# Optimization experiments

Hardware: AMD Instinct MI355X
Metric: run time of the kernel (lower is better)

## Reference

```python
import jax, jax.numpy as jnp
import numpy as np

NEG_INF = -1e9  # matches torch masked_fill value -1000000000.0
K = 3  # Conv1d kernel size


def setup_inputs() -> dict:
    key = jax.random.key(0)
    k1, k2, k3, k4 = jax.random.split(key, 4)
    B, V, F, H = 128, 200, 64, 128
    input_visit = jax.random.normal(k1, (B, V, F), dtype=jnp.float32)
    visit_mask = jax.random.randint(k2, (B, 1, V - K + 1), 0, 2, dtype=jnp.int32)
    # per-feature Conv1d(1, H, 3) weights stacked: [F, H, K], bias [F, H]
    fan_in = 1 * K
    bound = 1.0 / np.sqrt(fan_in)
    conv_w = jax.random.uniform(k3, (F, H, K), dtype=jnp.float32, minval=-bound, maxval=bound)
    conv_b = jax.random.uniform(k4, (F, H), dtype=jnp.float32, minval=-bound, maxval=bound)
    return {"input_visit": input_visit, "visit_mask": visit_mask, "conv_w": conv_w, "conv_b": conv_b}


def reference(input_visit, visit_mask, conv_w, conv_b):
    # input_visit: [B, V, F]; visit_mask: [B, 1, L] with L = V-K+1
    B, V, F = input_visit.shape
    L = V - K + 1
    x = jnp.transpose(input_visit, (0, 2, 1))  # [B, F, V]
    # sliding windows: [B, F, L, K]
    win = jnp.stack([x[:, :, k:k + L] for k in range(K)], axis=-1)
    # per-feature conv (in_channels=1): [B, F, H, L]
    conv = jnp.einsum('bflk,fhk->bfhl', win, conv_w) + conv_b[None, :, :, None]
    # masked_fill where mask == 0, broadcast [B,1,1,L] -> [B,F,H,L]
    masked = jnp.where(visit_mask[:, None, :, :] == 0, NEG_INF, conv)
    # max over time -> [B, F, H] (== torch.cat of per-feature outputs along dim=1)
    return jnp.max(masked, axis=-1)
```

## Files before the change

kernel.cpp:

```cpp
#include <hip/hip_runtime.h>


#define NEG_INF_F (-1e9f)

typedef float v2f __attribute__((ext_vector_type(2)));

constexpr int B_ = 128;
constexpr int V_ = 200;
constexpr int F_ = 64;
constexpr int H_ = 128;
constexpr int L_ = V_ - 3 + 1;

constexpr int NTHR = 256;
constexpr int FG   = 8;
constexpr int HPT  = 8;
constexpr int MAXW = (L_ + 7) & ~7;
constexpr int WSTR = 4 * MAXW + 8;

__global__ __launch_bounds__(NTHR)
void fve_kernel(const float* __restrict__ x,
                const int*   __restrict__ mask,
                const float* __restrict__ w,
                const float* __restrict__ bias,
                float* __restrict__ out)
{
    __shared__ __align__(16) float xc[FG][WSTR];
    __shared__ int vlist[L_];
    __shared__ int vcnt;

    const int b  = blockIdx.x >> 3;
    const int f0 = (blockIdx.x & 7) * FG;
    const int t  = threadIdx.x;

    if (t == 0) vcnt = 0;
    __syncthreads();

    if (t < L_ && mask[b * L_ + t] != 0) {
        const int p = atomicAdd(&vcnt, 1);
        vlist[p] = t;
    }
    __syncthreads();

    const int n    = vcnt;
    const int npad = (n + 7) & ~7;

    for (int item = t; item < npad * 8; item += NTHR) {
        const int j    = item >> 3;
        const int k    = (item >> 1) & 3;
        const int half = item & 1;
        if (k == 3) continue;
        const int l = (j < n) ? vlist[j] : vlist[0];
        const float4 g = *reinterpret_cast<const float4*>(
            x + ((size_t)b * V_ + l + k) * F_ + f0 + half * 4);
        const int col = 4 * j + k;
        xc[half * 4 + 0][col] = g.x;
        xc[half * 4 + 1][col] = g.y;
        xc[half * 4 + 2][col] = g.z;
        xc[half * 4 + 3][col] = g.w;
    }
    __syncthreads();

    const int f_local = t >> 5;
    const int f       = f0 + f_local;
    const int h_lane  = (t >> 1) & 15;
    const int h0      = h_lane * HPT;
    const int l_lane  = t & 1;

    const float* wp = w + ((size_t)f * H_ + h0) * 3;
    float wt[24];
#pragma unroll
    for (int j = 0; j < 6; ++j)
        *reinterpret_cast<float4*>(&wt[j * 4]) =
            *reinterpret_cast<const float4*>(wp + j * 4);

    float bsc[8];
    *reinterpret_cast<float4*>(&bsc[0]) =
        *reinterpret_cast<const float4*>(bias + (size_t)f * H_ + h0);
    *reinterpret_cast<float4*>(&bsc[4]) =
        *reinterpret_cast<const float4*>(bias + (size_t)f * H_ + h0 + 4);

    v2f wp0[4], wp1[4], wp2[4], bpk[4], mpk[4];
#pragma unroll
    for (int p = 0; p < 4; ++p) {
        wp0[p] = (v2f){wt[6 * p + 0], wt[6 * p + 3]};
        wp1[p] = (v2f){wt[6 * p + 1], wt[6 * p + 4]};
        wp2[p] = (v2f){wt[6 * p + 2], wt[6 * p + 5]};
        bpk[p] = (v2f){bsc[2 * p], bsc[2 * p + 1]};
        mpk[p] = (v2f){NEG_INF_F, NEG_INF_F};
    }

    const float4* xq = reinterpret_cast<const float4*>(&xc[f_local][0]);

#define PROCQ(Q)                                                              \
    do {                                                                      \
        const v2f X0 = (v2f){(Q).x, (Q).x};                                   \
        const v2f X1 = (v2f){(Q).y, (Q).y};                                   \
        const v2f X2 = (v2f){(Q).z, (Q).z};                                   \
        _Pragma("unroll")                                                     \
        for (int p = 0; p < 4; ++p) {                                         \
            const v2f c = __builtin_elementwise_fma(X0, wp0[p],               \
                          __builtin_elementwise_fma(X1, wp1[p],               \
                          __builtin_elementwise_fma(X2, wp2[p], bpk[p])));    \
            mpk[p] = __builtin_elementwise_max(mpk[p], c);                    \
        }                                                                     \
    } while (0)

    for (int u = 0; u < npad; u += 8) {
        const int i0 = u + l_lane;
        const float4 q0 = xq[i0];
        const float4 q1 = xq[i0 + 2];
        const float4 q2 = xq[i0 + 4];
        const float4 q3 = xq[i0 + 6];
        PROCQ(q0);
        PROCQ(q1);
        PROCQ(q2);
        PROCQ(q3);
    }
#undef PROCQ

#pragma unroll
    for (int p = 0; p < 4; ++p) {
        const float a = __shfl_xor(mpk[p].x, 1, 64);
        const float c = __shfl_xor(mpk[p].y, 1, 64);
        mpk[p].x = fmaxf(mpk[p].x, a);
        mpk[p].y = fmaxf(mpk[p].y, c);
    }

    float* op = out + ((size_t)b * F_ + f) * H_ + h0 + l_lane * 4;
    const int pb = l_lane * 2;
    *reinterpret_cast<float4*>(op) =
        make_float4(mpk[pb].x, mpk[pb].y, mpk[pb + 1].x, mpk[pb + 1].y);
}

extern "C" void kernel_launch(void* const* d_in, const int* in_sizes, int n_in,
                              void* d_out, int out_size, void* d_ws, size_t ws_size,
                              hipStream_t stream) {
    const float* x    = (const float*)d_in[0];
    const int*   mask = (const int*)d_in[1];
    const float* w    = (const float*)d_in[2];
    const float* bias = (const float*)d_in[3];
    float* out = (float*)d_out;

    const int grid = B_ * (F_ / FG);
    fve_kernel<<<grid, NTHR, 0, stream>>>(x, mask, w, bias, out);
}
```

Before: 16.20 us.

## Double features per block and h-outputs per thread for more register reuse

Each block now handles 16 features instead of 8, so the grid shrinks to 512 blocks and each gathered x window feeds more features. Each thread computes 16 h-channels instead of 8, so every LDS float4 load is reused across twice as many FMAs. Each wave now covers 4 features with 8 h-lanes and 2 l-lanes. The costs are more registers per thread, fewer blocks to spread across CUs, and more shared memory per block, all of which can lower occupancy.

```diff
diff --git a/kernel.cpp b/kernel.cpp
--- a/kernel.cpp
+++ b/kernel.cpp
@@ -12,8 +12,9 @@
 constexpr int L_ = V_ - 3 + 1;
 
 constexpr int NTHR = 256;
-constexpr int FG   = 8;
-constexpr int HPT  = 8;
+constexpr int FG   = 16;
+constexpr int NFW  = 4;
+constexpr int HPT  = 16;
 constexpr int MAXW = (L_ + 7) & ~7;
 constexpr int WSTR = 4 * MAXW + 8;
 
@@ -28,8 +29,8 @@
     __shared__ int vlist[L_];
     __shared__ int vcnt;
 
-    const int b  = blockIdx.x >> 3;
-    const int f0 = (blockIdx.x & 7) * FG;
+    const int b  = blockIdx.x >> 2;
+    const int f0 = (blockIdx.x & 3) * FG;
     const int t  = threadIdx.x;
 
     if (t == 0) vcnt = 0;
@@ -44,44 +45,47 @@
     const int n    = vcnt;
     const int npad = (n + 7) & ~7;
 
-    for (int item = t; item < npad * 8; item += NTHR) {
-        const int j    = item >> 3;
-        const int k    = (item >> 1) & 3;
-        const int half = item & 1;
+    for (int item = t; item < npad * 16; item += NTHR) {
+        const int j = item >> 4;
+        const int k = (item >> 2) & 3;
+        const int q = item & 3;
         if (k == 3) continue;
         const int l = (j < n) ? vlist[j] : vlist[0];
         const float4 g = *reinterpret_cast<const float4*>(
-            x + ((size_t)b * V_ + l + k) * F_ + f0 + half * 4);
+            x + ((size_t)b * V_ + l + k) * F_ + f0 + q * 4);
         const int col = 4 * j + k;
-        xc[half * 4 + 0][col] = g.x;
-        xc[half * 4 + 1][col] = g.y;
-        xc[half * 4 + 2][col] = g.z;
-        xc[half * 4 + 3][col] = g.w;
+        xc[4 * q + 0][col] = g.x;
+        xc[4 * q + 1][col] = g.y;
+        xc[4 * q + 2][col] = g.z;
+        xc[4 * q + 3][col] = g.w;
     }
     __syncthreads();
 
-    const int f_local = t >> 5;
+    const int wave    = t >> 6;
+    const int lane    = t & 63;
+    const int f_sub   = lane >> 4;
+    const int h_lane  = (lane >> 1) & 7;
+    const int l_lane  = lane & 1;
+    const int f_local = wave * NFW + f_sub;
     const int f       = f0 + f_local;
-    const int h_lane  = (t >> 1) & 15;
     const int h0      = h_lane * HPT;
-    const int l_lane  = t & 1;
 
     const float* wp = w + ((size_t)f * H_ + h0) * 3;
-    float wt[24];
+    float wt[48];
 #pragma unroll
-    for (int j = 0; j < 6; ++j)
+    for (int j = 0; j < 12; ++j)
         *reinterpret_cast<float4*>(&wt[j * 4]) =
             *reinterpret_cast<const float4*>(wp + j * 4);
 
-    float bsc[8];
-    *reinterpret_cast<float4*>(&bsc[0]) =
-        *reinterpret_cast<const float4*>(bias + (size_t)f * H_ + h0);
-    *reinterpret_cast<float4*>(&bsc[4]) =
-        *reinterpret_cast<const float4*>(bias + (size_t)f * H_ + h0 + 4);
+    float bsc[16];
+#pragma unroll
+    for (int j = 0; j < 4; ++j)
+        *reinterpret_cast<float4*>(&bsc[j * 4]) =
+            *reinterpret_cast<const float4*>(bias + (size_t)f * H_ + h0 + j * 4);
 
-    v2f wp0[4], wp1[4], wp2[4], bpk[4], mpk[4];
+    v2f wp0[8], wp1[8], wp2[8], bpk[8], mpk[8];
 #pragma unroll
-    for (int p = 0; p < 4; ++p) {
+    for (int p = 0; p < 8; ++p) {
         wp0[p] = (v2f){wt[6 * p + 0], wt[6 * p + 3]};
         wp1[p] = (v2f){wt[6 * p + 1], wt[6 * p + 4]};
         wp2[p] = (v2f){wt[6 * p + 2], wt[6 * p + 5]};
@@ -97,7 +101,7 @@
         const v2f X1 = (v2f){(Q).y, (Q).y};                                   \
         const v2f X2 = (v2f){(Q).z, (Q).z};                                   \
         _Pragma("unroll")                                                     \
-        for (int p = 0; p < 4; ++p) {                                         \
+        for (int p = 0; p < 8; ++p) {                                         \
             const v2f c = __builtin_elementwise_fma(X0, wp0[p],               \
                           __builtin_elementwise_fma(X1, wp1[p],               \
                           __builtin_elementwise_fma(X2, wp2[p], bpk[p])));    \
@@ -119,17 +123,19 @@
 #undef PROCQ
 
 #pragma unroll
-    for (int p = 0; p < 4; ++p) {
+    for (int p = 0; p < 8; ++p) {
         const float a = __shfl_xor(mpk[p].x, 1, 64);
         const float c = __shfl_xor(mpk[p].y, 1, 64);
         mpk[p].x = fmaxf(mpk[p].x, a);
         mpk[p].y = fmaxf(mpk[p].y, c);
     }
 
-    float* op = out + ((size_t)b * F_ + f) * H_ + h0 + l_lane * 4;
-    const int pb = l_lane * 2;
+    float* op = out + ((size_t)b * F_ + f) * H_ + h0 + l_lane * 8;
+    const int pb = l_lane * 4;
     *reinterpret_cast<float4*>(op) =
         make_float4(mpk[pb].x, mpk[pb].y, mpk[pb + 1].x, mpk[pb + 1].y);
+    *reinterpret_cast<float4*>(op + 4) =
+        make_float4(mpk[pb + 2].x, mpk[pb + 2].y, mpk[pb + 3].x, mpk[pb + 3].y);
 }
 
 extern "C" void kernel_launch(void* const* d_in, const int* in_sizes, int n_in,
```

After: 18.30 us. +13.0%, slower.

## Widen per-thread H tile, hoist weight loads, use ballot-based mask compaction

Applied to the files above, without the earlier changes.

Each thread now computes 16 output channels instead of 8, with four lanes splitting the time steps, so every shared-memory read of a window feeds twice as many FMAs. The weight and bias global loads are moved ahead of the first barrier so their latency overlaps the mask compaction. Mask compaction now uses a wavefront ballot plus one atomic per wave instead of one atomic per valid position. The trade-off is roughly double the per-thread register use, padding to 16 positions, and an extra shuffle round in the final max reduction.

```diff
diff --git a/kernel.cpp b/kernel.cpp
--- a/kernel.cpp
+++ b/kernel.cpp
@@ -13,9 +13,9 @@
 
 constexpr int NTHR = 256;
 constexpr int FG   = 8;
-constexpr int HPT  = 8;
-constexpr int MAXW = (L_ + 7) & ~7;
-constexpr int WSTR = 4 * MAXW + 8;
+constexpr int HPT  = 16;
+constexpr int MAXW = (L_ + 15) & ~15;
+constexpr int WSTR = 4 * MAXW + 16;
 
 __global__ __launch_bounds__(NTHR)
 void fve_kernel(const float* __restrict__ x,
@@ -25,24 +25,53 @@
                 float* __restrict__ out)
 {
     __shared__ __align__(16) float xc[FG][WSTR];
-    __shared__ int vlist[L_];
+    __shared__ int vlist[MAXW];
     __shared__ int vcnt;
 
     const int b  = blockIdx.x >> 3;
     const int f0 = (blockIdx.x & 7) * FG;
     const int t  = threadIdx.x;
+    const int lane = t & 63;
+
+    const int f_sub   = lane >> 5;
+    const int h_lane  = (lane >> 2) & 7;
+    const int l_lane  = lane & 3;
+    const int f_local = (t >> 6) * 2 + f_sub;
+    const int f       = f0 + f_local;
+    const int h0      = h_lane * HPT;
 
     if (t == 0) vcnt = 0;
+
+    const float* wp = w + ((size_t)f * H_ + h0) * 3;
+    float wt[48];
+#pragma unroll
+    for (int j = 0; j < 12; ++j)
+        *reinterpret_cast<float4*>(&wt[j * 4]) =
+            *reinterpret_cast<const float4*>(wp + j * 4);
+
+    float bsc[16];
+#pragma unroll
+    for (int j = 0; j < 4; ++j)
+        *reinterpret_cast<float4*>(&bsc[j * 4]) =
+            *reinterpret_cast<const float4*>(bias + (size_t)f * H_ + h0 + j * 4);
+
     __syncthreads();
 
-    if (t < L_ && mask[b * L_ + t] != 0) {
-        const int p = atomicAdd(&vcnt, 1);
-        vlist[p] = t;
+    {
+        const bool valid = (t < L_) && (mask[b * L_ + t] != 0);
+        const unsigned long long bal = __ballot(valid);
+        int base = 0;
+        if (lane == 0) base = atomicAdd(&vcnt, __popcll(bal));
+        base = __shfl(base, 0, 64);
+        if (valid) {
+            const int pos = base + (int)__popcll(bal & ((1ull << lane) - 1ull));
+            vlist[pos] = t;
+        }
     }
     __syncthreads();
 
     const int n    = vcnt;
-    const int npad = (n + 7) & ~7;
+    const int npad = (n + 15) & ~15;
 
     for (int item = t; item < npad * 8; item += NTHR) {
         const int j    = item >> 3;
@@ -60,28 +89,9 @@
     }
     __syncthreads();
 
-    const int f_local = t >> 5;
-    const int f       = f0 + f_local;
-    const int h_lane  = (t >> 1) & 15;
-    const int h0      = h_lane * HPT;
-    const int l_lane  = t & 1;
-
-    const float* wp = w + ((size_t)f * H_ + h0) * 3;
-    float wt[24];
+    v2f wp0[8], wp1[8], wp2[8], bpk[8], mpk[8];
 #pragma unroll
-    for (int j = 0; j < 6; ++j)
-        *reinterpret_cast<float4*>(&wt[j * 4]) =
-            *reinterpret_cast<const float4*>(wp + j * 4);
-
-    float bsc[8];
-    *reinterpret_cast<float4*>(&bsc[0]) =
-        *reinterpret_cast<const float4*>(bias + (size_t)f * H_ + h0);
-    *reinterpret_cast<float4*>(&bsc[4]) =
-        *reinterpret_cast<const float4*>(bias + (size_t)f * H_ + h0 + 4);
-
-    v2f wp0[4], wp1[4], wp2[4], bpk[4], mpk[4];
-#pragma unroll
-    for (int p = 0; p < 4; ++p) {
+    for (int p = 0; p < 8; ++p) {
         wp0[p] = (v2f){wt[6 * p + 0], wt[6 * p + 3]};
         wp1[p] = (v2f){wt[6 * p + 1], wt[6 * p + 4]};
         wp2[p] = (v2f){wt[6 * p + 2], wt[6 * p + 5]};
@@ -97,7 +107,7 @@
         const v2f X1 = (v2f){(Q).y, (Q).y};                                   \
         const v2f X2 = (v2f){(Q).z, (Q).z};                                   \
         _Pragma("unroll")                                                     \
-        for (int p = 0; p < 4; ++p) {                                         \
+        for (int p = 0; p < 8; ++p) {                                         \
             const v2f c = __builtin_elementwise_fma(X0, wp0[p],               \
                           __builtin_elementwise_fma(X1, wp1[p],               \
                           __builtin_elementwise_fma(X2, wp2[p], bpk[p])));    \
@@ -105,12 +115,12 @@
         }                                                                     \
     } while (0)
 
-    for (int u = 0; u < npad; u += 8) {
+    for (int u = 0; u < npad; u += 16) {
         const int i0 = u + l_lane;
         const float4 q0 = xq[i0];
-        const float4 q1 = xq[i0 + 2];
-        const float4 q2 = xq[i0 + 4];
-        const float4 q3 = xq[i0 + 6];
+        const float4 q1 = xq[i0 + 4];
+        const float4 q2 = xq[i0 + 8];
+        const float4 q3 = xq[i0 + 12];
         PROCQ(q0);
         PROCQ(q1);
         PROCQ(q2);
@@ -119,9 +129,13 @@
 #undef PROCQ
 
 #pragma unroll
-    for (int p = 0; p < 4; ++p) {
-        const float a = __shfl_xor(mpk[p].x, 1, 64);
-        const float c = __shfl_xor(mpk[p].y, 1, 64);
+    for (int p = 0; p < 8; ++p) {
+        float a = __shfl_xor(mpk[p].x, 1, 64);
+        float c = __shfl_xor(mpk[p].y, 1, 64);
+        mpk[p].x = fmaxf(mpk[p].x, a);
+        mpk[p].y = fmaxf(mpk[p].y, c);
+        a = __shfl_xor(mpk[p].x, 2, 64);
+        c = __shfl_xor(mpk[p].y, 2, 64);
         mpk[p].x = fmaxf(mpk[p].x, a);
         mpk[p].y = fmaxf(mpk[p].y, c);
     }
```

Result: slower. 18.31 us (+13.1%).

## Halve features per block, split time across four lanes, use ballot compaction

Applied to the files above, without the earlier changes.

Each block now handles 4 features instead of 8, which doubles the grid to 2048 blocks. Each wave owns one feature, and four lanes split the time axis between them, with a two-step shuffle max at the end. The shared-memory atomic compaction of valid timesteps is replaced by a wave ballot/popcount prefix scan, and launch bounds request 8 blocks per CU. The aim is more parallelism and occupancy plus a shorter per-thread serial loop. In exchange, each block reloads the weights and x rows, adds reduction shuffles, and half the lanes sit idle at the store.

```diff
diff --git a/kernel.cpp b/kernel.cpp
--- a/kernel.cpp
+++ b/kernel.cpp
@@ -12,12 +12,12 @@
 constexpr int L_ = V_ - 3 + 1;
 
 constexpr int NTHR = 256;
-constexpr int FG   = 8;
+constexpr int FG   = 4;
 constexpr int HPT  = 8;
 constexpr int MAXW = (L_ + 7) & ~7;
-constexpr int WSTR = 4 * MAXW + 8;
+constexpr int WSTR = 4 * MAXW + 16;
 
-__global__ __launch_bounds__(NTHR)
+__global__ __launch_bounds__(NTHR, 8)
 void fve_kernel(const float* __restrict__ x,
                 const int*   __restrict__ mask,
                 const float* __restrict__ w,
@@ -25,46 +25,53 @@
                 float* __restrict__ out)
 {
     __shared__ __align__(16) float xc[FG][WSTR];
-    __shared__ int vlist[L_];
-    __shared__ int vcnt;
+    __shared__ int vlist[MAXW];
+    __shared__ int wcount[4];
 
-    const int b  = blockIdx.x >> 3;
-    const int f0 = (blockIdx.x & 7) * FG;
-    const int t  = threadIdx.x;
+    const int b    = blockIdx.x >> 4;
+    const int f0   = (blockIdx.x & 15) * FG;
+    const int t    = threadIdx.x;
+    const int wave = t >> 6;
+    const int lane = t & 63;
 
-    if (t == 0) vcnt = 0;
-    __syncthreads();
-
-    if (t < L_ && mask[b * L_ + t] != 0) {
-        const int p = atomicAdd(&vcnt, 1);
-        vlist[p] = t;
+    {
+        const bool valid = (t < L_) && (mask[b * L_ + t] != 0);
+        const unsigned long long bal = __ballot(valid);
+        if (lane == 0) wcount[wave] = (int)__popcll(bal);
+        __syncthreads();
+        int base = 0;
+#pragma unroll
+        for (int ww = 0; ww < 4; ++ww)
+            if (ww < wave) base += wcount[ww];
+        if (valid) {
+            const int pos = base + (int)__popcll(bal & ((1ull << lane) - 1ull));
+            vlist[pos] = t;
+        }
     }
     __syncthreads();
 
-    const int n    = vcnt;
+    const int n    = wcount[0] + wcount[1] + wcount[2] + wcount[3];
     const int npad = (n + 7) & ~7;
 
-    for (int item = t; item < npad * 8; item += NTHR) {
-        const int j    = item >> 3;
-        const int k    = (item >> 1) & 3;
-        const int half = item & 1;
+    for (int item = t; item < npad * 4; item += NTHR) {
+        const int j = item >> 2;
+        const int k = item & 3;
         if (k == 3) continue;
         const int l = (j < n) ? vlist[j] : vlist[0];
         const float4 g = *reinterpret_cast<const float4*>(
-            x + ((size_t)b * V_ + l + k) * F_ + f0 + half * 4);
+            x + ((size_t)b * V_ + l + k) * F_ + f0);
         const int col = 4 * j + k;
-        xc[half * 4 + 0][col] = g.x;
-        xc[half * 4 + 1][col] = g.y;
-        xc[half * 4 + 2][col] = g.z;
-        xc[half * 4 + 3][col] = g.w;
+        xc[0][col] = g.x;
+        xc[1][col] = g.y;
+        xc[2][col] = g.z;
+        xc[3][col] = g.w;
     }
     __syncthreads();
 
-    const int f_local = t >> 5;
-    const int f       = f0 + f_local;
-    const int h_lane  = (t >> 1) & 15;
-    const int h0      = h_lane * HPT;
-    const int l_lane  = t & 1;
+    const int h_lane = (lane >> 2) & 15;
+    const int l_lane = lane & 3;
+    const int f      = f0 + wave;
+    const int h0     = h_lane * HPT;
 
     const float* wp = w + ((size_t)f * H_ + h0) * 3;
     float wt[24];
@@ -89,7 +96,7 @@
         mpk[p] = (v2f){NEG_INF_F, NEG_INF_F};
     }
 
-    const float4* xq = reinterpret_cast<const float4*>(&xc[f_local][0]);
+    const float4* xq = reinterpret_cast<const float4*>(&xc[wave][0]);
 
 #define PROCQ(Q)                                                              \
     do {                                                                      \
@@ -108,28 +115,30 @@
     for (int u = 0; u < npad; u += 8) {
         const int i0 = u + l_lane;
         const float4 q0 = xq[i0];
-        const float4 q1 = xq[i0 + 2];
-        const float4 q2 = xq[i0 + 4];
-        const float4 q3 = xq[i0 + 6];
+        const float4 q1 = xq[i0 + 4];
         PROCQ(q0);
         PROCQ(q1);
-        PROCQ(q2);
-        PROCQ(q3);
     }
 #undef PROCQ
 
 #pragma unroll
     for (int p = 0; p < 4; ++p) {
-        const float a = __shfl_xor(mpk[p].x, 1, 64);
-        const float c = __shfl_xor(mpk[p].y, 1, 64);
+        float a = __shfl_xor(mpk[p].x, 1, 64);
+        float c = __shfl_xor(mpk[p].y, 1, 64);
+        mpk[p].x = fmaxf(mpk[p].x, a);
+        mpk[p].y = fmaxf(mpk[p].y, c);
+        a = __shfl_xor(mpk[p].x, 2, 64);
+        c = __shfl_xor(mpk[p].y, 2, 64);
         mpk[p].x = fmaxf(mpk[p].x, a);
         mpk[p].y = fmaxf(mpk[p].y, c);
     }
 
-    float* op = out + ((size_t)b * F_ + f) * H_ + h0 + l_lane * 4;
-    const int pb = l_lane * 2;
-    *reinterpret_cast<float4*>(op) =
-        make_float4(mpk[pb].x, mpk[pb].y, mpk[pb + 1].x, mpk[pb + 1].y);
+    if (l_lane < 2) {
+        float* op = out + ((size_t)b * F_ + f) * H_ + h0 + l_lane * 4;
+        const int pb = l_lane * 2;
+        *reinterpret_cast<float4*>(op) =
+            make_float4(mpk[pb].x, mpk[pb].y, mpk[pb + 1].x, mpk[pb + 1].y);
+    }
 }
 
 extern "C" void kernel_launch(void* const* d_in, const int* in_sizes, int n_in,
```

After: 22.18 us. 37.0% more time.
